# Kernel tuning notes

Hardware: AMD Instinct MI355X
Metric: run time of the kernel (lower is better)

Reference implementation:

```python
import jax, jax.numpy as jnp
import numpy as np
import math

DIM = 1024
EPS = 1e-6

def rms_norm(x):
    return x * jax.lax.rsqrt(jnp.mean(x * x, axis=-1, keepdims=True) + EPS)

def setup_inputs() -> dict:
    key = jax.random.key(0)
    k1, k2, k3 = jax.random.split(key, 3)
    T, B, D = 512, 32, DIM
    x = jax.random.normal(k1, (T, B, D), dtype=jnp.float32)
    h0 = jnp.zeros((B, D), dtype=jnp.float32)
    # Parameters: W xavier-uniform, W_h ~ orthogonal-ish scaled by 0.01, b zeros
    bound = math.sqrt(6.0 / (D + D))
    W = jax.random.uniform(k2, (D, D), minval=-bound, maxval=bound, dtype=jnp.float32)
    W_h = 0.01 * jax.random.normal(k3, (D, D), dtype=jnp.float32) / math.sqrt(D)
    b = jnp.zeros((D,), dtype=jnp.float32)
    log_alpha = jnp.asarray(math.log(0.1), dtype=jnp.float32)
    log_beta = jnp.asarray(math.log(0.01), dtype=jnp.float32)
    return {"x": x, "h0": h0, "W": W, "W_h": W_h, "b": b,
            "log_alpha": log_alpha, "log_beta": log_beta}

def reference(x, h0, W, W_h, b, log_alpha, log_beta):
    alpha = jnp.exp(log_alpha)
    beta = jax.nn.sigmoid(log_beta) * 0.1
    # Precompute input projection for all timesteps: [T,B,D]
    Wx_all = jnp.einsum('tbd,ed->tbe', x, W) + b

    def step(h_prev, wx_t):
        h_new = h_prev + alpha * wx_t + beta * (h_prev @ W_h.T)
        h_new = rms_norm(h_new)
        out = h_new * jax.nn.silu(h_new)
        return h_new, (h_new, out)

    _, (hs, outs) = jax.lax.scan(step, h0, Wx_all)
    h = jnp.concatenate([h0[None], hs], axis=0)  # [T+1,B,D]
    return outs, h
```

## Files before the change

kernel.cpp:

```cpp
#include <hip/hip_runtime.h>
#include <stdint.h>

#define T_STEPS 512
#define BATCH   32
#define DIMN    1024
#define MROWS   (T_STEPS*BATCH)
#define BD      (BATCH*DIMN)

typedef _Float16 f16;
typedef _Float16 f16x8 __attribute__((ext_vector_type(8)));
typedef _Float16 f16x4 __attribute__((ext_vector_type(4)));
typedef _Float16 f16x2 __attribute__((ext_vector_type(2)));
typedef float    f32x4 __attribute__((ext_vector_type(4)));

union U8 { f16x8 v; f16x2 p[4]; };

__device__ __forceinline__ f16x2 pkrtz(float a, float b) {
  return __builtin_bit_cast(f16x2, __builtin_amdgcn_cvt_pkrtz(a, b));
}

__device__ __forceinline__ void load16_to_lds(const f16* gptr, f16* lptr) {
  __builtin_amdgcn_global_load_lds(
      (const __attribute__((address_space(1))) unsigned int*)(uintptr_t)gptr,
      (__attribute__((address_space(3))) unsigned int*)(uint32_t)(uintptr_t)lptr,
      16, 0, 0);
}

template<int CTRL>
__device__ __forceinline__ float dpp_ror_add(float v) {
  int iv = __float_as_int(v);
  int rv = __builtin_amdgcn_update_dpp(iv, iv, CTRL, 0xF, 0xF, false);
  return v + __int_as_float(rv);
}

__device__ __forceinline__ float wave_allsum(float s) {
  s = dpp_ror_add<0x128>(s);
  s = dpp_ror_add<0x124>(s);
  s = dpp_ror_add<0x122>(s);
  s = dpp_ror_add<0x121>(s);
  float a = __int_as_float(__builtin_amdgcn_readlane(__float_as_int(s), 0));
  float b = __int_as_float(__builtin_amdgcn_readlane(__float_as_int(s), 16));
  float c = __int_as_float(__builtin_amdgcn_readlane(__float_as_int(s), 32));
  float d = __int_as_float(__builtin_amdgcn_readlane(__float_as_int(s), 48));
  return (a + b) + (c + d);
}

__global__ __launch_bounds__(256) void cvt_f32_f16(const float* __restrict__ src,
                                                   f16* __restrict__ dst, int n8) {
  int i = blockIdx.x * 256 + threadIdx.x;
  if (i >= n8) return;
  const float4* s = (const float4*)src;
  float4 a = s[2*i], b = s[2*i + 1];
  f16x8 o = { (f16)a.x, (f16)a.y, (f16)a.z, (f16)a.w,
              (f16)b.x, (f16)b.y, (f16)b.z, (f16)b.w };
  *(f16x8*)(dst + (size_t)i * 8) = o;
}

__global__ __launch_bounds__(256) void gemm_bt_f16(
    const f16* __restrict__ A, const f16* __restrict__ B,
    const float* __restrict__ bias, f16* __restrict__ Cout,
    const float* __restrict__ la, const float* __restrict__ lb,
    const float* __restrict__ rowscale, const f16* __restrict__ addend, int mode) {
  constexpr int K = DIMN;
  constexpr int N = DIMN;
  __shared__ f16 Alds[128 * 32];
  __shared__ f16 Blds[128 * 32];
  const int tid  = threadIdx.x;
  const int lane = tid & 63;
  const int wid  = tid >> 6;
  const int wm = wid & 1, wn = wid >> 1;
  const int l15  = lane & 15;
  const int quad = lane >> 4;
  const int swz  = (l15 >> 1) & 3;
  const int rowBase = blockIdx.x * 128;
  const int colBase = blockIdx.y * 128;
  const int sr = lane >> 2;
  const int cs = lane & 3;

  const float scale = (mode == 0) ? expf(la[0])
                                  : 0.1f / (1.0f + expf(-lb[0]));

  f32x4 acc[4][4] = {};

  for (int k0 = 0; k0 < K; k0 += 32) {
    #pragma unroll
    for (int i = 0; i < 2; ++i) {
      const int g = wid + i * 4;
      const int r = g * 16 + sr;
      const int cd = cs ^ ((r >> 1) & 3);
      load16_to_lds(A + (size_t)(rowBase + r) * K + k0 + cd * 8, Alds + g * 512);
      load16_to_lds(B + (size_t)(colBase + r) * K + k0 + cd * 8, Blds + g * 512);
    }
    __syncthreads();
    f16x8 af[4], bf[4];
    #pragma unroll
    for (int mi = 0; mi < 4; ++mi) {
      const int r = wm * 64 + mi * 16 + l15;
      af[mi] = *(const f16x8*)(Alds + r * 32 + (quad ^ swz) * 8);
    }
    #pragma unroll
    for (int ni = 0; ni < 4; ++ni) {
      const int r = wn * 64 + ni * 16 + l15;
      bf[ni] = *(const f16x8*)(Blds + r * 32 + (quad ^ swz) * 8);
    }
    #pragma unroll
    for (int mi = 0; mi < 4; ++mi)
      #pragma unroll
      for (int ni = 0; ni < 4; ++ni)
        acc[mi][ni] = __builtin_amdgcn_mfma_f32_16x16x32_f16(af[mi], bf[ni], acc[mi][ni], 0, 0, 0);
    __syncthreads();
  }

  float colb[4];
  #pragma unroll
  for (int ni = 0; ni < 4; ++ni)
    colb[ni] = (mode == 0) ? bias[colBase + wn * 64 + ni * 16 + l15] : 0.0f;

  #pragma unroll
  for (int mi = 0; mi < 4; ++mi) {
    const int m0 = rowBase + wm * 64 + mi * 16 + quad * 4;
    #pragma unroll
    for (int j = 0; j < 4; ++j) {
      const size_t row = (size_t)(m0 + j);
      const float rs = (mode == 0) ? scale : scale * rowscale[row];
      #pragma unroll
      for (int ni = 0; ni < 4; ++ni) {
        const int n = colBase + wn * 64 + ni * 16 + l15;
        float v;
        if (mode == 0) v = rs * (acc[mi][ni][j] + colb[ni]);
        else           v = fmaf(rs, acc[mi][ni][j], (float)addend[row * N + n]);
        Cout[row * N + n] = (f16)v;
      }
    }
  }
}

template<int SHIFT>
__global__ __launch_bounds__(64) void scan_wave(
    const f16* __restrict__ Win,
    const float* __restrict__ h0,
    f16* __restrict__ G,
    float* __restrict__ S) {
  const int b = blockIdx.x;
  const int l = threadIdx.x;
  const size_t base = (size_t)b * DIMN + (size_t)l * 8;

  float u[16];
  {
    float4 a0 = *(const float4*)(h0 + base);
    float4 a1 = *(const float4*)(h0 + base + 4);
    float4 a2 = *(const float4*)(h0 + base + 512);
    float4 a3 = *(const float4*)(h0 + base + 516);
    u[0]=a0.x; u[1]=a0.y; u[2]=a0.z; u[3]=a0.w;
    u[4]=a1.x; u[5]=a1.y; u[6]=a1.z; u[7]=a1.w;
    u[8]=a2.x; u[9]=a2.y; u[10]=a2.z; u[11]=a2.w;
    u[12]=a3.x; u[13]=a3.y; u[14]=a3.z; u[15]=a3.w;
    if (SHIFT) {
      f16x8 g0, g1;
      #pragma unroll
      for (int i = 0; i < 8; ++i) { g0[i] = (f16)u[i]; g1[i] = (f16)u[i+8]; }
      *(f16x8*)(G + base) = g0;
      *(f16x8*)(G + base + 512) = g1;
      if (l == 0) S[b] = 1.0f;
    }
  }

  float c  = 1.0f;
  float ic = 1.0f;
  float kk = 1.0f / DIMN;

  U8 bw0[8], bw1[8];
  #pragma unroll
  for (int j = 0; j < 8; ++j) {
    bw0[j].v = *(const f16x8*)(Win + (size_t)j * BD + base);
    bw1[j].v = *(const f16x8*)(Win + (size_t)j * BD + base + 512);
  }

  for (int tb = 0; tb < T_STEPS; tb += 8) {
    #pragma unroll
    for (int j = 0; j < 8; ++j) {
      const int t = tb + j;
      U8 w0 = bw0[j], w1 = bw1[j];
      int tn = t + 8; if (tn > T_STEPS - 1) tn = T_STEPS - 1;
      bw0[j].v = *(const f16x8*)(Win + (size_t)tn * BD + base);
      bw1[j].v = *(const f16x8*)(Win + (size_t)tn * BD + base + 512);
      #pragma unroll
      for (int i = 0; i < 8; ++i) {
        u[i]   = fmaf(c, (float)w0.v[i], u[i]);
        u[i+8] = fmaf(c, (float)w1.v[i], u[i+8]);
      }
      float s0 = 0.f, s1 = 0.f, s2 = 0.f, s3 = 0.f;
      #pragma unroll
      for (int i = 0; i < 4; ++i) {
        s0 = fmaf(u[i],    u[i],    s0);
        s1 = fmaf(u[i+4],  u[i+4],  s1);
        s2 = fmaf(u[i+8],  u[i+8],  s2);
        s3 = fmaf(u[i+12], u[i+12], s3);
      }
      const float Q   = wave_allsum((s0 + s1) + (s2 + s3));
      const float m   = fmaf(Q, kk, 1e-6f);
      const float rho = __builtin_amdgcn_rsqf(m);
      c  = c * (m * rho);
      ic = ic * rho;
      kk = kk * (rho * rho);
      if (SHIFT == 0 || t < T_STEPS - 1) {
        U8 g0, g1;
        #pragma unroll
        for (int i = 0; i < 4; ++i) {
          g0.p[i] = pkrtz(u[2*i],   u[2*i+1]);
          g1.p[i] = pkrtz(u[2*i+8], u[2*i+9]);
        }
        const size_t off = (size_t)(t + SHIFT) * BD + base;
        *(f16x8*)(G + off) = g0.v;
        *(f16x8*)(G + off + 512) = g1.v;
        if (l == 0) S[(t + SHIFT) * BATCH + b] = ic;
      }
    }
  }
}

__global__ __launch_bounds__(256) void expand_kernel(
    const f16* __restrict__ G1, const float* __restrict__ S1v,
    const float* __restrict__ h0,
    float* __restrict__ outs, float* __restrict__ hout) {
  const long long total8 = (long long)T_STEPS * BD / 8;
  const long long idx = (long long)blockIdx.x * 256 + threadIdx.x;
  if (idx < total8) {
    const size_t e = (size_t)idx * 8;
    f16x8 g = *(const f16x8*)(G1 + e);
    const float s = S1v[e >> 10];
    float v[8], o[8];
    #pragma unroll
    for (int i = 0; i < 8; ++i) v[i] = (float)g[i] * s;
    #pragma unroll
    for (int i = 0; i < 8; ++i) o[i] = v[i] * v[i] / (1.0f + expf(-v[i]));
    *(float4*)(hout + BD + e)     = make_float4(v[0], v[1], v[2], v[3]);
    *(float4*)(hout + BD + e + 4) = make_float4(v[4], v[5], v[6], v[7]);
    *(float4*)(outs + e)     = make_float4(o[0], o[1], o[2], o[3]);
    *(float4*)(outs + e + 4) = make_float4(o[4], o[5], o[6], o[7]);
  } else {
    const size_t j = (size_t)(idx - total8) * 8;
    if (j < (size_t)BD) {
      float4 a0 = *(const float4*)(h0 + j);
      float4 a1 = *(const float4*)(h0 + j + 4);
      *(float4*)(hout + j)     = a0;
      *(float4*)(hout + j + 4) = a1;
    }
  }
}

extern "C" void kernel_launch(void* const* d_in, const int* in_sizes, int n_in,
                              void* d_out, int out_size, void* d_ws, size_t ws_size,
                              hipStream_t stream) {
  const float* x    = (const float*)d_in[0];
  const float* h0   = (const float*)d_in[1];
  const float* W    = (const float*)d_in[2];
  const float* Wh   = (const float*)d_in[3];
  const float* bias = (const float*)d_in[4];
  const float* la   = (const float*)d_in[5];
  const float* lb   = (const float*)d_in[6];

  char* ws = (char*)d_ws;
  f16* XH   = (f16*)(ws);
  f16* W16  = (f16*)(ws + 33554432ull);
  f16* WH16 = (f16*)(ws + 35651584ull);
  f16* WX16 = (f16*)(ws + 37748736ull);
  f16* G0   = (f16*)(ws + 71303168ull);
  f16* C16  = (f16*)(ws + 104857600ull);
  f16* G1   = XH;
  float* S0 = (float*)(ws + 33554432ull);
  float* S1 = (float*)(ws + 35651584ull);

  float* outs = (float*)d_out;
  float* hout = outs + (size_t)T_STEPS * BD;

  cvt_f32_f16<<<dim3((MROWS * DIMN / 8) / 256), 256, 0, stream>>>(x, XH, MROWS * DIMN / 8);
  cvt_f32_f16<<<dim3((DIMN * DIMN / 8) / 256), 256, 0, stream>>>(W, W16, DIMN * DIMN / 8);
  cvt_f32_f16<<<dim3((DIMN * DIMN / 8) / 256), 256, 0, stream>>>(Wh, WH16, DIMN * DIMN / 8);

  gemm_bt_f16<<<dim3(MROWS / 128, DIMN / 128), 256, 0, stream>>>(
      XH, W16, bias, WX16, la, lb, nullptr, nullptr, 0);

  scan_wave<1><<<dim3(BATCH), 64, 0, stream>>>(WX16, h0, G0, S0);

  gemm_bt_f16<<<dim3(MROWS / 128, DIMN / 128), 256, 0, stream>>>(
      G0, WH16, nullptr, C16, la, lb, S0, WX16, 1);

  scan_wave<0><<<dim3(BATCH), 64, 0, stream>>>(C16, h0, G1, S1);

  const int total8 = T_STEPS * BD / 8;
  expand_kernel<<<dim3(total8 / 256 + 16), 256, 0, stream>>>(G1, S1, h0, outs, hout);
}
```

Measured before the change: 582.5 us.

## Replace vector scans with Gram-matrix scalar scan and parallel recombine

Reformulates each sequential normalized scan so the per-step squared norm comes from a precomputed Gram matrix of the inputs (via MFMA) plus a projection against h0. A single-wave scalar recurrence then produces the per-step coefficients. Separate wider-grid kernels reconstruct the states in parallel and fuse the expand/silu output. This targets the serial latency of the 32-block vector scan, at the cost of extra Gram GEMMs, fp16 Gram precision risk, and row-scale indexing changed to a batch-major layout.

```diff
diff --git a/kernel.cpp b/kernel.cpp
--- a/kernel.cpp
+++ b/kernel.cpp
@@ -9,7 +9,6 @@
 
 typedef _Float16 f16;
 typedef _Float16 f16x8 __attribute__((ext_vector_type(8)));
-typedef _Float16 f16x4 __attribute__((ext_vector_type(4)));
 typedef _Float16 f16x2 __attribute__((ext_vector_type(2)));
 typedef float    f32x4 __attribute__((ext_vector_type(4)));
 
@@ -122,7 +121,9 @@
     #pragma unroll
     for (int j = 0; j < 4; ++j) {
       const size_t row = (size_t)(m0 + j);
-      const float rs = (mode == 0) ? scale : scale * rowscale[row];
+      const float rs = (mode == 0)
+          ? scale
+          : scale * rowscale[(((int)row & 31) << 9) | ((int)row >> 5)];
       #pragma unroll
       for (int ni = 0; ni < 4; ++ni) {
         const int n = colBase + wn * 64 + ni * 16 + l15;
@@ -135,116 +136,239 @@
   }
 }
 
+__global__ __launch_bounds__(256) void gram_f16(
+    const f16* __restrict__ A, f16* __restrict__ Gout) {
+  const int bx = blockIdx.x, by = blockIdx.y, bz = blockIdx.z;
+  if (by < bx) return;
+  __shared__ f16 Alds[128 * 32];
+  __shared__ f16 Blds[128 * 32];
+  const int tid  = threadIdx.x;
+  const int lane = tid & 63;
+  const int wid  = tid >> 6;
+  const int wm = wid & 1, wn = wid >> 1;
+  const int l15  = lane & 15;
+  const int quad = lane >> 4;
+  const int swz  = (l15 >> 1) & 3;
+  const int rowBase = bx * 128;
+  const int colBase = by * 128;
+  const int sr = lane >> 2;
+  const int cs = lane & 3;
+  const f16* Ab = A + (size_t)bz * DIMN;
+
+  f32x4 acc[4][4] = {};
+
+  for (int k0 = 0; k0 < DIMN; k0 += 32) {
+    #pragma unroll
+    for (int i = 0; i < 2; ++i) {
+      const int g = wid + i * 4;
+      const int r = g * 16 + sr;
+      const int cd = cs ^ ((r >> 1) & 3);
+      load16_to_lds(Ab + (size_t)(rowBase + r) * BD + k0 + cd * 8, Alds + g * 512);
+      load16_to_lds(Ab + (size_t)(colBase + r) * BD + k0 + cd * 8, Blds + g * 512);
+    }
+    __syncthreads();
+    f16x8 af[4], bf[4];
+    #pragma unroll
+    for (int mi = 0; mi < 4; ++mi) {
+      const int r = wm * 64 + mi * 16 + l15;
+      af[mi] = *(const f16x8*)(Alds + r * 32 + (quad ^ swz) * 8);
+    }
+    #pragma unroll
+    for (int ni = 0; ni < 4; ++ni) {
+      const int r = wn * 64 + ni * 16 + l15;
+      bf[ni] = *(const f16x8*)(Blds + r * 32 + (quad ^ swz) * 8);
+    }
+    #pragma unroll
+    for (int mi = 0; mi < 4; ++mi)
+      #pragma unroll
+      for (int ni = 0; ni < 4; ++ni)
+        acc[mi][ni] = __builtin_amdgcn_mfma_f32_16x16x32_f16(af[mi], bf[ni], acc[mi][ni], 0, 0, 0);
+    __syncthreads();
+  }
+
+  f16* Gb = Gout + (size_t)bz * (T_STEPS * T_STEPS);
+  #pragma unroll
+  for (int mi = 0; mi < 4; ++mi) {
+    const int m0 = rowBase + wm * 64 + mi * 16 + quad * 4;
+    #pragma unroll
+    for (int j = 0; j < 4; ++j) {
+      #pragma unroll
+      for (int ni = 0; ni < 4; ++ni) {
+        const int n = colBase + wn * 64 + ni * 16 + l15;
+        Gb[(size_t)(m0 + j) * T_STEPS + n] = (f16)acc[mi][ni][j];
+      }
+    }
+  }
+}
+
+__global__ __launch_bounds__(256) void gemv_p(
+    const f16* __restrict__ Wm, const float* __restrict__ h0,
+    float* __restrict__ P) {
+  const int b = blockIdx.x, sg = blockIdx.y;
+  const int w = threadIdx.x >> 6, l = threadIdx.x & 63;
+  float h[16];
+  {
+    const float* hp = h0 + (size_t)b * DIMN + l * 16;
+    #pragma unroll
+    for (int i = 0; i < 4; ++i) {
+      float4 a = *(const float4*)(hp + i * 4);
+      h[i*4+0] = a.x; h[i*4+1] = a.y; h[i*4+2] = a.z; h[i*4+3] = a.w;
+    }
+  }
+  for (int k = 0; k < 16; ++k) {
+    const int s = sg * 64 + w * 16 + k;
+    const f16* wp = Wm + (size_t)s * BD + (size_t)b * DIMN + l * 16;
+    f16x8 a0 = *(const f16x8*)(wp);
+    f16x8 a1 = *(const f16x8*)(wp + 8);
+    float acc = 0.f;
+    #pragma unroll
+    for (int i = 0; i < 8; ++i) acc = fmaf((float)a0[i], h[i], acc);
+    #pragma unroll
+    for (int i = 0; i < 8; ++i) acc = fmaf((float)a1[i], h[i+8], acc);
+    acc = wave_allsum(acc);
+    if (l == 0) P[(size_t)b * 512 + s] = acc;
+  }
+}
+
 template<int SHIFT>
-__global__ __launch_bounds__(64) void scan_wave(
-    const f16* __restrict__ Win,
+__global__ __launch_bounds__(64, 1) void scalar_scan(
+    const f16* __restrict__ Gm, const float* __restrict__ P,
     const float* __restrict__ h0,
-    f16* __restrict__ G,
-    float* __restrict__ S) {
-  const int b = blockIdx.x;
-  const int l = threadIdx.x;
-  const size_t base = (size_t)b * DIMN + (size_t)l * 8;
-
-  float u[16];
+    float* __restrict__ Carr, float* __restrict__ Sarr) {
+  const int b = blockIdx.x, l = threadIdx.x;
+  const f16* Gb = Gm + (size_t)b * (T_STEPS * T_STEPS);
+  float N;
   {
-    float4 a0 = *(const float4*)(h0 + base);
-    float4 a1 = *(const float4*)(h0 + base + 4);
-    float4 a2 = *(const float4*)(h0 + base + 512);
-    float4 a3 = *(const float4*)(h0 + base + 516);
-    u[0]=a0.x; u[1]=a0.y; u[2]=a0.z; u[3]=a0.w;
-    u[4]=a1.x; u[5]=a1.y; u[6]=a1.z; u[7]=a1.w;
-    u[8]=a2.x; u[9]=a2.y; u[10]=a2.z; u[11]=a2.w;
-    u[12]=a3.x; u[13]=a3.y; u[14]=a3.z; u[15]=a3.w;
-    if (SHIFT) {
-      f16x8 g0, g1;
+    const float* hp = h0 + (size_t)b * DIMN + l * 16;
+    float na = 0.f;
+    #pragma unroll
+    for (int i = 0; i < 4; ++i) {
+      float4 a = *(const float4*)(hp + i * 4);
+      na = fmaf(a.x, a.x, na); na = fmaf(a.y, a.y, na);
+      na = fmaf(a.z, a.z, na); na = fmaf(a.w, a.w, na);
+    }
+    N = wave_allsum(na);
+  }
+  float d[8];
+  {
+    float4 p0 = *(const float4*)(P + (size_t)b * 512 + l * 8);
+    float4 p1 = *(const float4*)(P + (size_t)b * 512 + l * 8 + 4);
+    d[0]=p0.x; d[1]=p0.y; d[2]=p0.z; d[3]=p0.w;
+    d[4]=p1.x; d[5]=p1.y; d[6]=p1.z; d[7]=p1.w;
+  }
+  float gd[8];
+  #pragma unroll
+  for (int j = 0; j < 8; ++j)
+    gd[j] = (float)Gb[(size_t)(l * 8 + j) * T_STEPS + (l * 8 + j)];
+  f16x8 grow[8];
+  #pragma unroll
+  for (int j = 0; j < 8; ++j)
+    grow[j] = *(const f16x8*)(Gb + (size_t)j * T_STEPS + l * 8);
+
+  float c = 1.f, ic = 1.f, kk = 1.f / DIMN;
+  if (SHIFT && l == 0) Sarr[(size_t)b * 512] = 1.f;
+  float ccap = 1.f, iccap = 1.f;
+
+  for (int tb = 0; tb < T_STEPS; tb += 8) {
+    const int a = tb >> 3;
+    #pragma unroll
+    for (int J = 0; J < 8; ++J) {
+      const int t = tb + J;
+      f16x8 g = grow[J];
+      int tn = t + 8; if (tn > T_STEPS - 1) tn = T_STEPS - 1;
+      grow[J] = *(const f16x8*)(Gb + (size_t)tn * T_STEPS + l * 8);
+      const float e   = __int_as_float(__builtin_amdgcn_readlane(__float_as_int(d[J]),  a));
+      const float gtt = __int_as_float(__builtin_amdgcn_readlane(__float_as_int(gd[J]), a));
+      const float cold = c;
       #pragma unroll
-      for (int i = 0; i < 8; ++i) { g0[i] = (f16)u[i]; g1[i] = (f16)u[i+8]; }
-      *(f16x8*)(G + base) = g0;
-      *(f16x8*)(G + base + 512) = g1;
-      if (l == 0) S[b] = 1.0f;
-    }
-  }
-
-  float c  = 1.0f;
-  float ic = 1.0f;
-  float kk = 1.0f / DIMN;
-
-  U8 bw0[8], bw1[8];
-  #pragma unroll
-  for (int j = 0; j < 8; ++j) {
-    bw0[j].v = *(const f16x8*)(Win + (size_t)j * BD + base);
-    bw1[j].v = *(const f16x8*)(Win + (size_t)j * BD + base + 512);
-  }
-
-  for (int tb = 0; tb < T_STEPS; tb += 8) {
-    #pragma unroll
-    for (int j = 0; j < 8; ++j) {
-      const int t = tb + j;
-      U8 w0 = bw0[j], w1 = bw1[j];
-      int tn = t + 8; if (tn > T_STEPS - 1) tn = T_STEPS - 1;
-      bw0[j].v = *(const f16x8*)(Win + (size_t)tn * BD + base);
-      bw1[j].v = *(const f16x8*)(Win + (size_t)tn * BD + base + 512);
-      #pragma unroll
-      for (int i = 0; i < 8; ++i) {
-        u[i]   = fmaf(c, (float)w0.v[i], u[i]);
-        u[i+8] = fmaf(c, (float)w1.v[i], u[i+8]);
-      }
-      float s0 = 0.f, s1 = 0.f, s2 = 0.f, s3 = 0.f;
-      #pragma unroll
-      for (int i = 0; i < 4; ++i) {
-        s0 = fmaf(u[i],    u[i],    s0);
-        s1 = fmaf(u[i+4],  u[i+4],  s1);
-        s2 = fmaf(u[i+8],  u[i+8],  s2);
-        s3 = fmaf(u[i+12], u[i+12], s3);
-      }
-      const float Q   = wave_allsum((s0 + s1) + (s2 + s3));
-      const float m   = fmaf(Q, kk, 1e-6f);
+      for (int j2 = 0; j2 < 8; ++j2) d[j2] = fmaf(cold, (float)g[j2], d[j2]);
+      N = fmaf(2.f * cold, e, fmaf(cold * cold, gtt, N));
+      const float m   = fmaf(N, kk, 1e-6f);
       const float rho = __builtin_amdgcn_rsqf(m);
-      c  = c * (m * rho);
+      c  = cold * (m * rho);
       ic = ic * rho;
       kk = kk * (rho * rho);
-      if (SHIFT == 0 || t < T_STEPS - 1) {
-        U8 g0, g1;
-        #pragma unroll
-        for (int i = 0; i < 4; ++i) {
-          g0.p[i] = pkrtz(u[2*i],   u[2*i+1]);
-          g1.p[i] = pkrtz(u[2*i+8], u[2*i+9]);
-        }
-        const size_t off = (size_t)(t + SHIFT) * BD + base;
-        *(f16x8*)(G + off) = g0.v;
-        *(f16x8*)(G + off + 512) = g1.v;
-        if (l == 0) S[(t + SHIFT) * BATCH + b] = ic;
-      }
-    }
-  }
-}
-
-__global__ __launch_bounds__(256) void expand_kernel(
-    const f16* __restrict__ G1, const float* __restrict__ S1v,
-    const float* __restrict__ h0,
+      ccap  = (l == J) ? cold : ccap;
+      iccap = (l == J) ? ic   : iccap;
+    }
+    if (l < 8) {
+      Carr[(size_t)b * 512 + tb + l] = ccap;
+      const int sidx = tb + SHIFT + l;
+      if (sidx < T_STEPS) Sarr[(size_t)b * 512 + sidx] = iccap;
+    }
+  }
+}
+
+__global__ __launch_bounds__(64) void recombine0(
+    const f16* __restrict__ Wx, const float* __restrict__ h0,
+    const float* __restrict__ Carr, f16* __restrict__ G0) {
+  const int b = blockIdx.x, dc = blockIdx.y, l = threadIdx.x;
+  const size_t base = (size_t)b * DIMN + dc * 128 + l * 2;
+  float u0 = h0[base], u1 = h0[base + 1];
+  *(f16x2*)(G0 + base) = pkrtz(u0, u1);
+  f16x2 wbuf[8];
+  #pragma unroll
+  for (int j = 0; j < 8; ++j) wbuf[j] = *(const f16x2*)(Wx + (size_t)j * BD + base);
+  const float* Cb = Carr + (size_t)b * 512;
+  for (int tb = 0; tb < T_STEPS; tb += 8) {
+    float4 ca = *(const float4*)(Cb + tb);
+    float4 cz = *(const float4*)(Cb + tb + 4);
+    const float cc[8] = {ca.x, ca.y, ca.z, ca.w, cz.x, cz.y, cz.z, cz.w};
+    #pragma unroll
+    for (int J = 0; J < 8; ++J) {
+      const int t = tb + J;
+      f16x2 w = wbuf[J];
+      int tn = t + 8; if (tn > T_STEPS - 1) tn = T_STEPS - 1;
+      wbuf[J] = *(const f16x2*)(Wx + (size_t)tn * BD + base);
+      u0 = fmaf(cc[J], (float)w[0], u0);
+      u1 = fmaf(cc[J], (float)w[1], u1);
+      if (t < T_STEPS - 1)
+        *(f16x2*)(G0 + (size_t)(t + 1) * BD + base) = pkrtz(u0, u1);
+    }
+  }
+}
+
+__global__ __launch_bounds__(64) void recombine1_expand(
+    const f16* __restrict__ Cin, const float* __restrict__ h0,
+    const float* __restrict__ Carr, const float* __restrict__ Sarr,
     float* __restrict__ outs, float* __restrict__ hout) {
-  const long long total8 = (long long)T_STEPS * BD / 8;
-  const long long idx = (long long)blockIdx.x * 256 + threadIdx.x;
-  if (idx < total8) {
-    const size_t e = (size_t)idx * 8;
-    f16x8 g = *(const f16x8*)(G1 + e);
-    const float s = S1v[e >> 10];
-    float v[8], o[8];
-    #pragma unroll
-    for (int i = 0; i < 8; ++i) v[i] = (float)g[i] * s;
-    #pragma unroll
-    for (int i = 0; i < 8; ++i) o[i] = v[i] * v[i] / (1.0f + expf(-v[i]));
-    *(float4*)(hout + BD + e)     = make_float4(v[0], v[1], v[2], v[3]);
-    *(float4*)(hout + BD + e + 4) = make_float4(v[4], v[5], v[6], v[7]);
-    *(float4*)(outs + e)     = make_float4(o[0], o[1], o[2], o[3]);
-    *(float4*)(outs + e + 4) = make_float4(o[4], o[5], o[6], o[7]);
-  } else {
-    const size_t j = (size_t)(idx - total8) * 8;
-    if (j < (size_t)BD) {
-      float4 a0 = *(const float4*)(h0 + j);
-      float4 a1 = *(const float4*)(h0 + j + 4);
-      *(float4*)(hout + j)     = a0;
-      *(float4*)(hout + j + 4) = a1;
+  const int b = blockIdx.x, dc = blockIdx.y, l = threadIdx.x;
+  if (dc == 8) {
+    const size_t o = (size_t)b * DIMN + (size_t)l * 16;
+    #pragma unroll
+    for (int i = 0; i < 4; ++i) {
+      float4 a = *(const float4*)(h0 + o + i * 4);
+      *(float4*)(hout + o + i * 4) = a;
+    }
+    return;
+  }
+  const size_t base = (size_t)b * DIMN + dc * 128 + l * 2;
+  float u0 = h0[base], u1 = h0[base + 1];
+  f16x2 wbuf[8];
+  #pragma unroll
+  for (int j = 0; j < 8; ++j) wbuf[j] = *(const f16x2*)(Cin + (size_t)j * BD + base);
+  const float* Cb = Carr + (size_t)b * 512;
+  const float* Sb = Sarr + (size_t)b * 512;
+  for (int tb = 0; tb < T_STEPS; tb += 8) {
+    float4 ca = *(const float4*)(Cb + tb);
+    float4 cz = *(const float4*)(Cb + tb + 4);
+    float4 sa = *(const float4*)(Sb + tb);
+    float4 sz = *(const float4*)(Sb + tb + 4);
+    const float cc[8] = {ca.x, ca.y, ca.z, ca.w, cz.x, cz.y, cz.z, cz.w};
+    const float ss[8] = {sa.x, sa.y, sa.z, sa.w, sz.x, sz.y, sz.z, sz.w};
+    #pragma unroll
+    for (int J = 0; J < 8; ++J) {
+      const int t = tb + J;
+      f16x2 w = wbuf[J];
+      int tn = t + 8; if (tn > T_STEPS - 1) tn = T_STEPS - 1;
+      wbuf[J] = *(const f16x2*)(Cin + (size_t)tn * BD + base);
+      u0 = fmaf(cc[J], (float)w[0], u0);
+      u1 = fmaf(cc[J], (float)w[1], u1);
+      const float v0 = ss[J] * u0, v1 = ss[J] * u1;
+      const float o0 = v0 * v0 / (1.f + expf(-v0));
+      const float o1 = v1 * v1 / (1.f + expf(-v1));
+      *(float2*)(outs + (size_t)t * BD + base) = make_float2(o0, o1);
+      *(float2*)(hout + (size_t)(t + 1) * BD + base) = make_float2(v0, v1);
     }
   }
 }
@@ -262,14 +386,18 @@
 
   char* ws = (char*)d_ws;
   f16* XH   = (f16*)(ws);
+  f16* GRAM = (f16*)(ws);
   f16* W16  = (f16*)(ws + 33554432ull);
   f16* WH16 = (f16*)(ws + 35651584ull);
   f16* WX16 = (f16*)(ws + 37748736ull);
   f16* G0   = (f16*)(ws + 71303168ull);
   f16* C16  = (f16*)(ws + 104857600ull);
-  f16* G1   = XH;
   float* S0 = (float*)(ws + 33554432ull);
+  float* C0 = (float*)(ws + 33554432ull + 65536ull);
+  float* P0 = (float*)(ws + 33554432ull + 131072ull);
   float* S1 = (float*)(ws + 35651584ull);
+  float* C1 = (float*)(ws + 35651584ull + 65536ull);
+  float* P1 = (float*)(ws + 35651584ull + 131072ull);
 
   float* outs = (float*)d_out;
   float* hout = outs + (size_t)T_STEPS * BD;
@@ -281,13 +409,16 @@
   gemm_bt_f16<<<dim3(MROWS / 128, DIMN / 128), 256, 0, stream>>>(
       XH, W16, bias, WX16, la, lb, nullptr, nullptr, 0);
 
-  scan_wave<1><<<dim3(BATCH), 64, 0, stream>>>(WX16, h0, G0, S0);
+  gram_f16<<<dim3(4, 4, BATCH), 256, 0, stream>>>(WX16, GRAM);
+  gemv_p<<<dim3(BATCH, 8), 256, 0, stream>>>(WX16, h0, P0);
+  scalar_scan<1><<<dim3(BATCH), 64, 0, stream>>>(GRAM, P0, h0, C0, S0);
+  recombine0<<<dim3(BATCH, 8), 64, 0, stream>>>(WX16, h0, C0, G0);
 
   gemm_bt_f16<<<dim3(MROWS / 128, DIMN / 128), 256, 0, stream>>>(
       G0, WH16, nullptr, C16, la, lb, S0, WX16, 1);
 
-  scan_wave<0><<<dim3(BATCH), 64, 0, stream>>>(C16, h0, G1, S1);
-
-  const int total8 = T_STEPS * BD / 8;
-  expand_kernel<<<dim3(total8 / 256 + 16), 256, 0, stream>>>(G1, S1, h0, outs, hout);
-}
+  gram_f16<<<dim3(4, 4, BATCH), 256, 0, stream>>>(C16, GRAM);
+  gemv_p<<<dim3(BATCH, 8), 256, 0, stream>>>(C16, h0, P1);
+  scalar_scan<0><<<dim3(BATCH), 64, 0, stream>>>(GRAM, P1, h0, C1, S1);
+  recombine1_expand<<<dim3(BATCH, 9), 64, 0, stream>>>(C16, h0, C1, S1, outs, hout);
+}
```

New measurement: 626.1 us. 7.5% more time.
